# Optimization experiments

Measured on AMD Instinct MI355X. Metric: run time of the kernel, lower is better.

The kernel has to match this reference:

```python
import jax, jax.numpy as jnp
import numpy as np

T, B, D, H = 512, 512, 512, 512

def setup_inputs() -> dict:
    key = jax.random.key(0)
    k_in, k_wih, k_whh, k_bih, k_bhh = jax.random.split(key, 5)
    s = 1.0 / np.sqrt(H)  # torch RNNCell init scale
    return {
        "inputs": jax.random.normal(k_in, (T, B, D), dtype=jnp.float32),
        "W_ih": jax.random.uniform(k_wih, (H, D), jnp.float32, -s, s),
        "W_hh": jax.random.uniform(k_whh, (H, H), jnp.float32, -s, s),
        "b_ih": jax.random.uniform(k_bih, (H,), jnp.float32, -s, s),
        "b_hh": jax.random.uniform(k_bhh, (H,), jnp.float32, -s, s),
        "hidden_size": H,
    }

def reference(inputs, W_ih, W_hh, b_ih, b_hh, hidden_size):
    # h_{t+1} = tanh(x_t @ W_ih^T + b_ih + h_t @ W_hh^T + b_hh)
    # Original inits hidden with inputs.shape[0] rows (quirk: requires T == B).
    h0 = jnp.zeros((inputs.shape[0], hidden_size), dtype=inputs.dtype)
    # Precompute the input projection for all steps in one big GEMM;
    # the recurrence itself must remain sequential.
    xp = jnp.einsum("tbd,hd->tbh", inputs, W_ih) + b_ih + b_hh  # [T, B, H]

    def step(h, xp_t):
        h = jnp.tanh(xp_t + h @ W_hh.T)
        return h, None

    h_final, _ = jax.lax.scan(step, h0, xp)
    return h_final
```

## Files before the change

### kernel.cpp

```cpp
#include <hip/hip_runtime.h>
#include <stdint.h>

#define TSTEPS 512
#define NB 512
#define ND 512
#define NH 512

#define NGROUPS 32
#define CELL_STRIDE 64

typedef _Float16 half8 __attribute__((ext_vector_type(8)));
typedef float float4v __attribute__((ext_vector_type(4)));

__device__ __forceinline__ float fast_tanh(float x) {
  float e = __expf(2.0f * x);
  return 1.0f - 2.0f * __builtin_amdgcn_rcpf(e + 1.0f);
}

__global__ void __launch_bounds__(256, 1)
rnn_persistent(const float* __restrict__ x,
               const float* __restrict__ Wih,
               const float* __restrict__ Whh,
               const float* __restrict__ bih,
               const float* __restrict__ bhh,
               float* __restrict__ out,
               _Float16* __restrict__ hbuf,
               unsigned* __restrict__ flags)
{
  __shared__ __attribute__((aligned(16))) float red[4][16][68];

  const int bid  = blockIdx.x;
  const int grp  = bid & 31;
  const int cwg  = bid >> 5;
  const int wave = threadIdx.x >> 6;
  const int lane = threadIdx.x & 63;
  const int m    = lane & 15;
  const int quad = lane >> 4;
  const int tid  = threadIdx.x;

  const int R     = grp * 16;
  const int C0    = cwg * 64;
  const int kbase = wave * 128;

  unsigned* gflags = flags + (size_t)grp * 8 * CELL_STRIDE;
  unsigned* myflag = gflags + cwg * CELL_STRIDE;
  const unsigned* pollcell = gflags + ((wave << 1) | (lane & 1)) * CELL_STRIDE;

  half8 wih_f[4][4];
  half8 whh_f[4][4];
  #pragma unroll
  for (int tile = 0; tile < 4; ++tile) {
    const int n = C0 + tile * 16 + m;
    const float* wr_ih = Wih + (size_t)n * ND;
    const float* wr_hh = Whh + (size_t)n * NH;
    #pragma unroll
    for (int kk = 0; kk < 4; ++kk) {
      const int k0 = kbase + kk * 32 + quad * 8;
      half8 a, b;
      #pragma unroll
      for (int j = 0; j < 8; ++j) {
        a[j] = (_Float16)wr_ih[k0 + j];
        b[j] = (_Float16)wr_hh[k0 + j];
      }
      wih_f[kk][tile] = a;
      whh_f[kk][tile] = b;
    }
  }

  const int prow = tid >> 4;
  const int pcol = (tid & 15) * 4;
  float4v bias4;
  #pragma unroll
  for (int j = 0; j < 4; ++j)
    bias4[j] = bih[C0 + pcol + j] + bhh[C0 + pcol + j];

  const int myrow = R + m;
  const int orow  = quad * 4;

  float4v xvA[4][2], xvB[4][2];
  {
    const float* xrow0 = x + (size_t)myrow * ND + kbase + quad * 8;
    #pragma unroll
    for (int kk = 0; kk < 4; ++kk) {
      xvA[kk][0] = *(const float4v*)(xrow0 + kk * 32);
      xvA[kk][1] = *(const float4v*)(xrow0 + kk * 32 + 4);
    }
  }

#define STEP(T, XU, XP)                                                        \
  {                                                                            \
    const int t_ = (T);                                                        \
    float4v acc[4];                                                            \
    _Pragma("unroll")                                                          \
    for (int tile = 0; tile < 4; ++tile) acc[tile] = (float4v){0.f,0.f,0.f,0.f};\
                       \
    _Pragma("unroll")                                                          \
    for (int kk = 0; kk < 4; ++kk) {                                           \
      half8 a;                                                                 \
      _Pragma("unroll")                                                        \
      for (int j = 0; j < 4; ++j) {                                            \
        a[j]     = (_Float16)XU[kk][0][j];                                     \
        a[j + 4] = (_Float16)XU[kk][1][j];                                     \
      }                                                                        \
      _Pragma("unroll")                                                        \
      for (int tile = 0; tile < 4; ++tile)                                     \
        acc[tile] = __builtin_amdgcn_mfma_f32_16x16x32_f16(a, wih_f[kk][tile], acc[tile], 0, 0, 0); \
    }                                                                          \
         \
    {                                                                          \
      const int tn_ = (t_ + 1 < TSTEPS) ? (t_ + 1) : t_;                       \
      const float* xrow_ = x + ((size_t)tn_ * NB + myrow) * ND + kbase + quad * 8; \
      _Pragma("unroll")                                                        \
      for (int kk = 0; kk < 4; ++kk) {                                         \
        XP[kk][0] = *(const float4v*)(xrow_ + kk * 32);                        \
        XP[kk][1] = *(const float4v*)(xrow_ + kk * 32 + 4);                    \
      }                                                                        \
    }                                                                          \
          \
    if (t_ > 0) {                                                              \
      const unsigned tgt = (unsigned)t_;                                       \
      unsigned v;                                                              \
      for (;;) {                                                               \
        v = __hip_atomic_load(pollcell, __ATOMIC_RELAXED, __HIP_MEMORY_SCOPE_AGENT); \
        if (__all((int)(v >= tgt))) break;                                     \
        __builtin_amdgcn_s_sleep(1);                                           \
      }                                                                        \
        \
      const unsigned v2 = (unsigned)__shfl_xor((int)v, 1, 64);                 \
      const _Float16* hb = hbuf + (size_t)(t_ & 1) * NB * NH + (size_t)((v | v2) >> 31); \
      const unsigned long long* hrow =                                         \
          (const unsigned long long*)(hb + (size_t)myrow * NH + kbase + quad * 8); \
      _Pragma("unroll")                                                        \
      for (int kk = 0; kk < 4; ++kk) {                                         \
        unsigned long long lo = __hip_atomic_load(hrow + kk * 8,     __ATOMIC_RELAXED, __HIP_MEMORY_SCOPE_AGENT); \
        unsigned long long hi = __hip_atomic_load(hrow + kk * 8 + 1, __ATOMIC_RELAXED, __HIP_MEMORY_SCOPE_AGENT); \
        union { unsigned long long u[2]; half8 h; } cv;                        \
        cv.u[0] = lo; cv.u[1] = hi;                                            \
        _Pragma("unroll")                                                      \
        for (int tile = 0; tile < 4; ++tile)                                   \
          acc[tile] = __builtin_amdgcn_mfma_f32_16x16x32_f16(cv.h, whh_f[kk][tile], acc[tile], 0, 0, 0); \
      }                                                                        \
    }                                                                          \
                                           \
    _Pragma("unroll")                                                          \
    for (int tile = 0; tile < 4; ++tile) {                                     \
      _Pragma("unroll")                                                        \
      for (int r = 0; r < 4; ++r)                                              \
        red[wave][orow + r][tile * 16 + m] = acc[tile][r];                     \
    }                                                                          \
    __syncthreads();                                           \
    float4v s = bias4;                                                         \
    _Pragma("unroll")                                                          \
    for (int w = 0; w < 4; ++w) {                                              \
      const float4v vv = *(const float4v*)&red[w][prow][pcol];                 \
      s[0] += vv[0]; s[1] += vv[1]; s[2] += vv[2]; s[3] += vv[3];              \
    }                                                                          \
    float4v o;                                                                 \
    _Pragma("unroll")                                                          \
    for (int j = 0; j < 4; ++j) o[j] = fast_tanh(s[j]);                        \
    if (t_ < TSTEPS - 1) {                                                     \
      _Float16* hb1 = hbuf + (size_t)((t_ + 1) & 1) * NB * NH;                 \
      union { _Float16 h[4]; unsigned long long u; } pk;                       \
      _Pragma("unroll")                                                        \
      for (int j = 0; j < 4; ++j) pk.h[j] = (_Float16)o[j];                    \
      __hip_atomic_store(                                                      \
          (unsigned long long*)(hb1 + (size_t)(R + prow) * NH + C0 + pcol),    \
          pk.u, __ATOMIC_RELAXED, __HIP_MEMORY_SCOPE_AGENT);                   \
        \
      asm volatile("s_waitcnt vmcnt(0)" ::: "memory");                         \
      __syncthreads();   \
      if (tid == 0)                                                            \
        __hip_atomic_store(myflag, (unsigned)(t_ + 1), __ATOMIC_RELAXED, __HIP_MEMORY_SCOPE_AGENT); \
    } else {                                                                   \
      *(float4v*)(out + (size_t)(R + prow) * NH + C0 + pcol) = o;              \
    }                                                                          \
  }

  for (int t = 0; t < TSTEPS; t += 2) {
    STEP(t,     xvA, xvB);
    STEP(t + 1, xvB, xvA);
  }
#undef STEP
}

extern "C" void kernel_launch(void* const* d_in, const int* in_sizes, int n_in,
                              void* d_out, int out_size, void* d_ws, size_t ws_size,
                              hipStream_t stream) {
  const float* x   = (const float*)d_in[0];
  const float* Wih = (const float*)d_in[1];
  const float* Whh = (const float*)d_in[2];
  const float* bih = (const float*)d_in[3];
  const float* bhh = (const float*)d_in[4];
  float* out = (float*)d_out;

  _Float16* hbuf  = (_Float16*)d_ws;
  unsigned* flags = (unsigned*)((char*)d_ws + (size_t)2 * NB * NH * 2);

  (void)hipMemsetAsync(flags, 0,
                       (size_t)NGROUPS * 8 * CELL_STRIDE * sizeof(unsigned),
                       stream);

  rnn_persistent<<<dim3(256), dim3(256), 0, stream>>>(
      x, Wih, Whh, bih, bhh, out, hbuf, flags);
}
```

Measured before the change: 2.193 ms.

## Replace flag-based step sync with sentinel-tagged data polling on 4-deep h ring

Drops the per-workgroup step flags and the second barrier before the flag store. Consumers now poll the hidden-state words themselves until no 64-bit word equals an all-ones sentinel. Producers clear slots two steps ahead on a four-deep ring buffer, and the reduction LDS is double-buffered so one barrier per step suffices. This removes a flag round trip and a __syncthreads from the critical path, but it depends on an fp16 tanh output never packing to all-ones and on relaxed-ordering correctness between the sentinel reset and the consumers.

```diff
diff --git a/kernel.cpp b/kernel.cpp
--- a/kernel.cpp
+++ b/kernel.cpp
@@ -5,17 +5,35 @@
 #define NB 512
 #define ND 512
 #define NH 512
-
-#define NGROUPS 32
-#define CELL_STRIDE 64
+#define SENT 0xFFFFFFFFFFFFFFFFull
 
 typedef _Float16 half8 __attribute__((ext_vector_type(8)));
 typedef float float4v __attribute__((ext_vector_type(4)));
+typedef unsigned long long u64;
 
 __device__ __forceinline__ float fast_tanh(float x) {
   float e = __expf(2.0f * x);
   return 1.0f - 2.0f * __builtin_amdgcn_rcpf(e + 1.0f);
 }
+
+#define AL(p)    __hip_atomic_load((p), __ATOMIC_RELAXED, __HIP_MEMORY_SCOPE_AGENT)
+#define AS(p, v) __hip_atomic_store((p), (v), __ATOMIC_RELAXED, __HIP_MEMORY_SCOPE_AGENT)
+
+#define LDSBAR()                                                               \
+  do {                                                                         \
+    asm volatile("s_waitcnt lgkmcnt(0)" ::: "memory");                         \
+    __builtin_amdgcn_s_barrier();                                              \
+  } while (0)
+
+#define PREFETCH_X(XP, TN)                                                     \
+  do {                                                                         \
+    const float* xrow_ = x + ((size_t)(TN) * NB + myrow) * ND + kbase + quad * 8; \
+    _Pragma("unroll")                                                          \
+    for (int kk = 0; kk < 4; ++kk) {                                           \
+      XP[kk][0] = *(const float4v*)(xrow_ + kk * 32);                          \
+      XP[kk][1] = *(const float4v*)(xrow_ + kk * 32 + 4);                      \
+    }                                                                          \
+  } while (0)
 
 __global__ void __launch_bounds__(256, 1)
 rnn_persistent(const float* __restrict__ x,
@@ -24,10 +42,9 @@
                const float* __restrict__ bih,
                const float* __restrict__ bhh,
                float* __restrict__ out,
-               _Float16* __restrict__ hbuf,
-               unsigned* __restrict__ flags)
+               _Float16* __restrict__ hbuf)
 {
-  __shared__ __attribute__((aligned(16))) float red[4][16][68];
+  __shared__ __attribute__((aligned(16))) float red[2][4][16][68];
 
   const int bid  = blockIdx.x;
   const int grp  = bid & 31;
@@ -41,10 +58,6 @@
   const int R     = grp * 16;
   const int C0    = cwg * 64;
   const int kbase = wave * 128;
-
-  unsigned* gflags = flags + (size_t)grp * 8 * CELL_STRIDE;
-  unsigned* myflag = gflags + cwg * CELL_STRIDE;
-  const unsigned* pollcell = gflags + ((wave << 1) | (lane & 1)) * CELL_STRIDE;
 
   half8 wih_f[4][4];
   half8 whh_f[4][4];
@@ -87,13 +100,19 @@
     }
   }
 
-#define STEP(T, XU, XP)                                                        \
+#define STEP(T, PAR, XU, XP)                                                   \
   {                                                                            \
     const int t_ = (T);                                                        \
+        \
+    if (t_ >= 2) {                                                             \
+      u64* cl = (u64*)(hbuf + (size_t)((t_ + 2) & 3) * NB * NH +               \
+                       (size_t)(R + prow) * NH + C0 + pcol);                   \
+      AS(cl, SENT);                                                            \
+    }                                                                          \
     float4v acc[4];                                                            \
     _Pragma("unroll")                                                          \
     for (int tile = 0; tile < 4; ++tile) acc[tile] = (float4v){0.f,0.f,0.f,0.f};\
-                       \
+                                         \
     _Pragma("unroll")                                                          \
     for (int kk = 0; kk < 4; ++kk) {                                           \
       half8 a;                                                                 \
@@ -106,79 +125,80 @@
       for (int tile = 0; tile < 4; ++tile)                                     \
         acc[tile] = __builtin_amdgcn_mfma_f32_16x16x32_f16(a, wih_f[kk][tile], acc[tile], 0, 0, 0); \
     }                                                                          \
-         \
-    {                                                                          \
+    if (t_ > 0) {                                                              \
       const int tn_ = (t_ + 1 < TSTEPS) ? (t_ + 1) : t_;                       \
-      const float* xrow_ = x + ((size_t)tn_ * NB + myrow) * ND + kbase + quad * 8; \
-      _Pragma("unroll")                                                        \
-      for (int kk = 0; kk < 4; ++kk) {                                         \
-        XP[kk][0] = *(const float4v*)(xrow_ + kk * 32);                        \
-        XP[kk][1] = *(const float4v*)(xrow_ + kk * 32 + 4);                    \
+      const _Float16* hb = hbuf + (size_t)(t_ & 3) * NB * NH;                  \
+      const u64* hrow = (const u64*)(hb + (size_t)myrow * NH + kbase + quad * 8); \
+                                           \
+      u64 w0 = AL(hrow + 0), w1 = AL(hrow + 1);                                \
+      u64 w2 = AL(hrow + 8), w3 = AL(hrow + 9);                                \
+      u64 w4 = AL(hrow + 16), w5 = AL(hrow + 17);                              \
+      u64 w6 = AL(hrow + 24), w7 = AL(hrow + 25);                              \
+      PREFETCH_X(XP, tn_);                                                     \
+      for (;;) {                                                               \
+        bool ok = (w0 != SENT) & (w1 != SENT) & (w2 != SENT) & (w3 != SENT) &  \
+                  (w4 != SENT) & (w5 != SENT) & (w6 != SENT) & (w7 != SENT);   \
+        if (__all((int)ok)) break;                                             \
+        __builtin_amdgcn_s_sleep(1);           \
+        w0 = AL(hrow + 0); w1 = AL(hrow + 1);                                  \
+        w2 = AL(hrow + 8); w3 = AL(hrow + 9);                                  \
+        w4 = AL(hrow + 16); w5 = AL(hrow + 17);                                \
+        w6 = AL(hrow + 24); w7 = AL(hrow + 25);                                \
       }                                                                        \
-    }                                                                          \
-          \
-    if (t_ > 0) {                                                              \
-      const unsigned tgt = (unsigned)t_;                                       \
-      unsigned v;                                                              \
-      for (;;) {                                                               \
-        v = __hip_atomic_load(pollcell, __ATOMIC_RELAXED, __HIP_MEMORY_SCOPE_AGENT); \
-        if (__all((int)(v >= tgt))) break;                                     \
-        __builtin_amdgcn_s_sleep(1);                                           \
-      }                                                                        \
-        \
-      const unsigned v2 = (unsigned)__shfl_xor((int)v, 1, 64);                 \
-      const _Float16* hb = hbuf + (size_t)(t_ & 1) * NB * NH + (size_t)((v | v2) >> 31); \
-      const unsigned long long* hrow =                                         \
-          (const unsigned long long*)(hb + (size_t)myrow * NH + kbase + quad * 8); \
-      _Pragma("unroll")                                                        \
-      for (int kk = 0; kk < 4; ++kk) {                                         \
-        unsigned long long lo = __hip_atomic_load(hrow + kk * 8,     __ATOMIC_RELAXED, __HIP_MEMORY_SCOPE_AGENT); \
-        unsigned long long hi = __hip_atomic_load(hrow + kk * 8 + 1, __ATOMIC_RELAXED, __HIP_MEMORY_SCOPE_AGENT); \
-        union { unsigned long long u[2]; half8 h; } cv;                        \
-        cv.u[0] = lo; cv.u[1] = hi;                                            \
-        _Pragma("unroll")                                                      \
-        for (int tile = 0; tile < 4; ++tile)                                   \
-          acc[tile] = __builtin_amdgcn_mfma_f32_16x16x32_f16(cv.h, whh_f[kk][tile], acc[tile], 0, 0, 0); \
-      }                                                                        \
-    }                                                                          \
-                                           \
+      union { u64 u[2]; half8 h; } cvv;                                        \
+      cvv.u[0] = w0; cvv.u[1] = w1;                                            \
+      _Pragma("unroll")                                                        \
+      for (int tile = 0; tile < 4; ++tile)                                     \
+        acc[tile] = __builtin_amdgcn_mfma_f32_16x16x32_f16(cvv.h, whh_f[0][tile], acc[tile], 0, 0, 0); \
+      cvv.u[0] = w2; cvv.u[1] = w3;                                            \
+      _Pragma("unroll")                                                        \
+      for (int tile = 0; tile < 4; ++tile)                                     \
+        acc[tile] = __builtin_amdgcn_mfma_f32_16x16x32_f16(cvv.h, whh_f[1][tile], acc[tile], 0, 0, 0); \
+      cvv.u[0] = w4; cvv.u[1] = w5;                                            \
+      _Pragma("unroll")                                                        \
+      for (int tile = 0; tile < 4; ++tile)                                     \
+        acc[tile] = __builtin_amdgcn_mfma_f32_16x16x32_f16(cvv.h, whh_f[2][tile], acc[tile], 0, 0, 0); \
+      cvv.u[0] = w6; cvv.u[1] = w7;                                            \
+      _Pragma("unroll")                                                        \
+      for (int tile = 0; tile < 4; ++tile)                                     \
+        acc[tile] = __builtin_amdgcn_mfma_f32_16x16x32_f16(cvv.h, whh_f[3][tile], acc[tile], 0, 0, 0); \
+    } else {                                                                   \
+      PREFETCH_X(XP, 1);                                                       \
+    }                                                                          \
+                       \
     _Pragma("unroll")                                                          \
     for (int tile = 0; tile < 4; ++tile) {                                     \
       _Pragma("unroll")                                                        \
       for (int r = 0; r < 4; ++r)                                              \
-        red[wave][orow + r][tile * 16 + m] = acc[tile][r];                     \
-    }                                                                          \
-    __syncthreads();                                           \
+        red[PAR][wave][orow + r][tile * 16 + m] = acc[tile][r];                \
+    }                                                                          \
+    LDSBAR();    \
     float4v s = bias4;                                                         \
     _Pragma("unroll")                                                          \
     for (int w = 0; w < 4; ++w) {                                              \
-      const float4v vv = *(const float4v*)&red[w][prow][pcol];                 \
+      const float4v vv = *(const float4v*)&red[PAR][w][prow][pcol];            \
       s[0] += vv[0]; s[1] += vv[1]; s[2] += vv[2]; s[3] += vv[3];              \
     }                                                                          \
     float4v o;                                                                 \
     _Pragma("unroll")                                                          \
     for (int j = 0; j < 4; ++j) o[j] = fast_tanh(s[j]);                        \
     if (t_ < TSTEPS - 1) {                                                     \
-      _Float16* hb1 = hbuf + (size_t)((t_ + 1) & 1) * NB * NH;                 \
-      union { _Float16 h[4]; unsigned long long u; } pk;                       \
+      u64* dst = (u64*)(hbuf + (size_t)((t_ + 1) & 3) * NB * NH +              \
+                        (size_t)(R + prow) * NH + C0 + pcol);                  \
+      union { _Float16 h[4]; u64 u; } pk;                                      \
       _Pragma("unroll")                                                        \
       for (int j = 0; j < 4; ++j) pk.h[j] = (_Float16)o[j];                    \
-      __hip_atomic_store(                                                      \
-          (unsigned long long*)(hb1 + (size_t)(R + prow) * NH + C0 + pcol),    \
-          pk.u, __ATOMIC_RELAXED, __HIP_MEMORY_SCOPE_AGENT);                   \
-        \
+                                                \
       asm volatile("s_waitcnt vmcnt(0)" ::: "memory");                         \
-      __syncthreads();   \
-      if (tid == 0)                                                            \
-        __hip_atomic_store(myflag, (unsigned)(t_ + 1), __ATOMIC_RELAXED, __HIP_MEMORY_SCOPE_AGENT); \
+      AS(dst, pk.u);                                                           \
     } else {                                                                   \
       *(float4v*)(out + (size_t)(R + prow) * NH + C0 + pcol) = o;              \
     }                                                                          \
   }
 
   for (int t = 0; t < TSTEPS; t += 2) {
-    STEP(t,     xvA, xvB);
-    STEP(t + 1, xvB, xvA);
+    STEP(t,     0, xvA, xvB);
+    STEP(t + 1, 1, xvB, xvA);
   }
 #undef STEP
 }
@@ -193,13 +213,10 @@
   const float* bhh = (const float*)d_in[4];
   float* out = (float*)d_out;
 
-  _Float16* hbuf  = (_Float16*)d_ws;
-  unsigned* flags = (unsigned*)((char*)d_ws + (size_t)2 * NB * NH * 2);
-
-  (void)hipMemsetAsync(flags, 0,
-                       (size_t)NGROUPS * 8 * CELL_STRIDE * sizeof(unsigned),
-                       stream);
+  _Float16* hbuf = (_Float16*)d_ws;
+
+  (void)hipMemsetAsync(hbuf, 0xFF, (size_t)4 * NB * NH * sizeof(_Float16), stream);
 
   rnn_persistent<<<dim3(256), dim3(256), 0, stream>>>(
-      x, Wih, Whh, bih, bhh, out, hbuf, flags);
+      x, Wih, Whh, bih, bhh, out, hbuf);
 }
```

Result: faster. 2.149 ms (-2.0%).
